# Kernel tuning notes

Measured on AMD Instinct MI355X. Metric: run time of the kernel, lower is better.

## Reference

```python
import jax, jax.numpy as jnp
import numpy as np
import math

N, E, G = 16000, 128000, 64
D, H, O, L, HID = 64, 4, 64, 5, 128
EPS = 1e-5

def _ln(x, g, b):
    mu = x.mean(-1, keepdims=True)
    var = ((x - mu) ** 2).mean(-1, keepdims=True)
    return (x - mu) / jnp.sqrt(var + EPS) * g + b

def _softplus_b64(x):
    # torch nn.Softplus(beta=64, threshold=64): x if 64*x > 64 else log1p(exp(64*x))/64
    z = jnp.minimum(x * 64.0, 64.0)
    return jnp.where(x * 64.0 > 64.0, x, jnp.log1p(jnp.exp(z)) / 64.0)

def setup_inputs() -> dict:
    key = jax.random.key(0)
    ks = jax.random.split(key, 32)
    s = 0.05
    d = {
        'x': jax.random.normal(ks[0], (N, 4), jnp.float32),
        'edge_attr': jax.random.normal(ks[1], (E, 9), jnp.float32),
        'edge_index': jax.random.randint(ks[2], (2, E), 0, N),
        'batch': jnp.sort(jax.random.randint(ks[3], (N,), 0, G)),
        'W_atom': jax.random.normal(ks[4], (4, D)) * s, 'b_atom': jnp.zeros((D,)),
        'We1': jax.random.normal(ks[5], (9, D)) * s, 'be1': jnp.zeros((D,)),
        'We2': jax.random.normal(ks[6], (D, D)) * s, 'be2': jnp.zeros((D,)),
        'Wq': jax.random.normal(ks[7], (L, D, H * O)) * s, 'bq': jnp.zeros((L, H * O)),
        'Wk': jax.random.normal(ks[8], (L, D, H * O)) * s, 'bk': jnp.zeros((L, H * O)),
        'Wv': jax.random.normal(ks[9], (L, D, H * O)) * s, 'bv': jnp.zeros((L, H * O)),
        'Wedge': jax.random.normal(ks[10], (L, D, H * O)) * s, 'bedge': jnp.zeros((L, H * O)),
        'Wfea': jax.random.normal(ks[11], (L, D, O)) * s, 'bfea': jnp.zeros((L, O)),
        'Wcat': jax.random.normal(ks[12], (L, H * O, O)) * s, 'bcat': jnp.zeros((L, O)),
        'Wupd': jax.random.normal(ks[13], (L, 3 * O, 3 * O)) * s, 'bupd': jnp.zeros((L, 3 * O)),
        'Wmsg': jax.random.normal(ks[14], (L, 3 * O, O)) * s, 'bmsg': jnp.zeros((L, O)),
        'g_msg': jnp.ones((L, O)), 'be_msg': jnp.zeros((L, O)),
        'g_ln': jnp.ones((L, 3 * O)), 'be_ln': jnp.zeros((L, 3 * O)),
        'g_bn': jnp.ones((L, O)), 'be_bn': jnp.zeros((L, O)),
        'Wfc': jax.random.normal(ks[15], (D, HID)) * s, 'bfc': jnp.zeros((HID,)),
        'Wout': jax.random.normal(ks[16], (HID, 1)) * s, 'bout': jnp.zeros((1,)),
    }
    return d

def _forward(x, edge_attr, W_atom, b_atom, We1, be1, We2, be2, Wq, bq, Wk, bk, Wv, bv,
             Wedge, bedge, Wfea, bfea, Wcat, bcat, Wupd, bupd, Wmsg, bmsg,
             g_msg, be_msg, g_ln, be_ln, g_bn, be_bn, Wfc, bfc, Wout, bout,
             edge_index, batch):
    src, dst = edge_index[0], edge_index[1]  # x_j = src, x_i = dst (flow source_to_target)
    h = x @ W_atom + b_atom  # [N, D]
    e = _softplus_b64(edge_attr @ We1 + be1) @ We2 + be2  # [E, D]
    scale = 1.0 / math.sqrt(3.0 * O)
    for l in range(L):
        Q = (h @ Wq[l] + bq[l]).reshape(N, H, O)
        K = (h @ Wk[l] + bk[l]).reshape(N, H, O)
        V = (h @ Wv[l] + bv[l]).reshape(N, H, O)
        Eh = (e @ Wedge[l] + bedge[l]).reshape(E, H, O)
        Qi = Q[dst]
        q_ij = jnp.concatenate([Qi, Qi, Qi], axis=-1)                 # [E, H, 3O]
        k_ij = jnp.concatenate([K[dst], K[src], Eh], axis=-1)
        v_ij = jnp.concatenate([V[dst], V[src], Eh], axis=-1)
        alpha = q_ij * k_ij * scale
        gate = jax.nn.sigmoid(_ln(alpha, g_ln[l], be_ln[l]))
        m = gate * (v_ij @ Wupd[l] + bupd[l])
        m = _ln(m @ Wmsg[l] + bmsg[l], g_msg[l], be_msg[l])           # [E, H, O]
        agg = jax.ops.segment_sum(m, dst, num_segments=N).reshape(N, H * O)
        out = agg @ Wcat[l] + bcat[l]
        mu = out.mean(0)
        var = ((out - mu) ** 2).mean(0)  # biased var, BN training mode
        out = (out - mu) / jnp.sqrt(var + EPS) * g_bn[l] + be_bn[l]
        h = jax.nn.silu(out) + (h @ Wfea[l] + bfea[l])
    ones = jnp.ones((N,), h.dtype)
    cnt = jax.ops.segment_sum(ones, batch, num_segments=G)
    pooled = jax.ops.segment_sum(h, batch, num_segments=G) / jnp.maximum(cnt, 1.0)[:, None]
    z = jax.nn.silu(pooled @ Wfc + bfc)
    return z @ Wout + bout  # [G, 1]

def reference(x, edge_attr, edge_index, batch, W_atom, b_atom, We1, be1, We2, be2,
              Wq, bq, Wk, bk, Wv, bv, Wedge, bedge, Wfea, bfea, Wcat, bcat,
              Wupd, bupd, Wmsg, bmsg, g_msg, be_msg, g_ln, be_ln, g_bn, be_bn,
              Wfc, bfc, Wout, bout):
    return _forward(x, edge_attr, W_atom, b_atom, We1, be1, We2, be2, Wq, bq, Wk, bk,
                    Wv, bv, Wedge, bedge, Wfea, bfea, Wcat, bcat, Wupd, bupd,
                    Wmsg, bmsg, g_msg, be_msg, g_ln, be_ln, g_bn, be_bn,
                    Wfc, bfc, Wout, bout, edge_index, batch)
```

## Files before the change

kernel.cpp:

```cpp
#include <hip/hip_runtime.h>
#include <hip/hip_bf16.h>
#include <math.h>

#define N_NODES 16000
#define N_EDGES 128000
#define N_GRAPH 64
#define NL 5
#define EPSV 1e-5f
#define SCALE 0.07216878364870323f

#define PCK 2048
#define ECOLS 1024
#define TILE 16
#define SWZ(r) (((r) & 7) << 2)

typedef __hip_bfloat16 bf16;
typedef __attribute__((ext_vector_type(8))) short short8;
typedef __attribute__((ext_vector_type(4))) short s4v;
typedef __attribute__((ext_vector_type(4))) float f32x4;
union S8U { short8 v; s4v h[2]; };

__device__ __forceinline__ ushort f2b(float x) {
    union { float f; uint u; } v; v.f = x;
    uint r = v.u + 0x7fffu + ((v.u >> 16) & 1u);
    return (ushort)(r >> 16);
}
__device__ __forceinline__ float b2fu(ushort u) { union { uint u; float f; } v; v.u = (uint)u << 16; return v.f; }
__device__ __forceinline__ float b2f_lo32(uint u) { union { uint u; float f; } v; v.u = u << 16; return v.f; }
__device__ __forceinline__ float b2f_hi32(uint u) { union { uint u; float f; } v; v.u = u & 0xffff0000u; return v.f; }

__global__ void pack_w(const float* __restrict__ Wq, const float* __restrict__ Wk,
                       const float* __restrict__ Wv, const float* __restrict__ Wupd,
                       const float* __restrict__ Wedge,
                       short* __restrict__ Wnp, short* __restrict__ Wep) {
    int idx = blockIdx.x * 256 + threadIdx.x;
    int total = NL * 64 * (PCK + ECOLS);
    if (idx >= total) return;
    int c = idx % (PCK + ECOLS);
    int k = (idx / (PCK + ECOLS)) % 64;
    int l = idx / (64 * (PCK + ECOLS));
    if (c < PCK) {
        int blk = c >> 10, hd = (c >> 8) & 3, ch = (c >> 2) & 63, j = c & 3;
        float v;
        if (blk == 0) {
            if (j == 0) v = Wq[(l*64 + k)*256 + hd*64 + ch];
            else {
                int p = (j - 1)*64 + ch;
                float s = 0.f;
                for (int q = 0; q < 64; ++q)
                    s += Wv[(l*64 + k)*256 + hd*64 + q] * Wupd[(l*192 + q)*192 + p];
                v = s;
            }
        } else {
            if (j == 0) v = Wk[(l*64 + k)*256 + hd*64 + ch];
            else {
                int p = (j - 1)*64 + ch;
                float s = 0.f;
                for (int q = 0; q < 64; ++q)
                    s += Wv[(l*64 + k)*256 + hd*64 + q] * Wupd[(l*192 + 64 + q)*192 + p];
                v = s;
            }
        }
        int t = c >> 4, s = k >> 5, lane = (c & 15) | (((k & 31) >> 3) << 4), jj = k & 7;
        size_t fo = ((size_t)(t*2 + s)*64 + lane)*8 + jj;
        ushort hi = f2b(v);
        ushort lo = f2b(v - b2fu(hi));
        Wnp[(size_t)l*2*64*PCK + fo] = (short)hi;
        Wnp[(size_t)l*2*64*PCK + (size_t)64*PCK + fo] = (short)lo;
    } else {
        int ce = c - PCK;
        float v;
        if (ce < 256) v = Wedge[(l*64 + k)*256 + ce];
        else {
            int cc = ce - 256, hd = cc / 192, p = cc % 192;
            float s = 0.f;
            for (int q = 0; q < 64; ++q)
                s += Wedge[(l*64 + k)*256 + hd*64 + q] * Wupd[(l*192 + 128 + q)*192 + p];
            v = s;
        }
        int t = ce >> 4, s = k >> 5, lane = (ce & 15) | (((k & 31) >> 3) << 4), jj = k & 7;
        size_t fo = ((size_t)(t*2 + s)*64 + lane)*8 + jj;
        ushort hi = f2b(v);
        ushort lo = f2b(v - b2fu(hi));
        Wep[(size_t)l*2*64*ECOLS + fo] = (short)hi;
        Wep[(size_t)l*2*64*ECOLS + (size_t)64*ECOLS + fo] = (short)lo;
    }
}

__global__ void pack_wmsg(const float* __restrict__ Wmsg, short* __restrict__ Wmf) {
    int idx = blockIdx.x * 256 + threadIdx.x;
    if (idx >= NL*192*64) return;
    int col = idx & 63, k = (idx >> 6) % 192, l = idx / (192*64);
    float v = Wmsg[(size_t)(l*192 + k)*64 + col];
    int t = col >> 4, s = k >> 5, lane = (col & 15) | (((k & 31) >> 3) << 4), j = k & 7;
    size_t fo = ((size_t)((t*6 + s)*64) + lane)*8 + j;
    ushort hi = f2b(v);
    ushort lo = f2b(v - b2fu(hi));
    Wmf[(size_t)l*2*12288 + fo] = (short)hi;
    Wmf[(size_t)l*2*12288 + 12288 + fo] = (short)lo;
}

__global__ void pack_b(const float* __restrict__ bq, const float* __restrict__ bk,
                       const float* __restrict__ bv, const float* __restrict__ Wupd,
                       const float* __restrict__ bupd, const float* __restrict__ bedge,
                       float* __restrict__ bnp, float* __restrict__ bep) {
    int idx = blockIdx.x * 256 + threadIdx.x;
    int total = NL * (PCK + ECOLS);
    if (idx >= total) return;
    int c = idx % (PCK + ECOLS);
    int l = idx / (PCK + ECOLS);
    if (c < PCK) {
        int blk = c >> 10, hd = (c >> 8) & 3, ch = (c >> 2) & 63, j = c & 3;
        float v;
        if (blk == 0) {
            if (j == 0) v = bq[l*256 + hd*64 + ch];
            else {
                int p = (j - 1)*64 + ch;
                float s = 0.f;
                for (int k = 0; k < 64; ++k) s += bv[l*256 + hd*64 + k] * Wupd[(l*192 + k)*192 + p];
                v = s;
            }
        } else {
            if (j == 0) v = bk[l*256 + hd*64 + ch];
            else {
                int p = (j - 1)*64 + ch;
                float s = 0.f;
                for (int k = 0; k < 64; ++k) s += bv[l*256 + hd*64 + k] * Wupd[(l*192 + 64 + k)*192 + p];
                v = s;
            }
        }
        bnp[l*PCK + c] = v;
    } else {
        int ce = c - PCK;
        float v;
        if (ce < 256) v = bedge[l*256 + ce];
        else {
            int cc = ce - 256, hd = cc / 192, p = cc % 192;
            float s = bupd[l*192 + p];
            for (int k = 0; k < 64; ++k) s += bedge[l*256 + hd*64 + k] * Wupd[(l*192 + 128 + k)*192 + p];
            v = s;
        }
        bep[l*ECOLS + ce] = v;
    }
}

__global__ void hist_k(const int* __restrict__ ei, int* __restrict__ hist) {
    int e = blockIdx.x * 256 + threadIdx.x;
    if (e < N_EDGES) atomicAdd(&hist[ei[N_EDGES + e]], 1);
}

__global__ void scan_k(const int* __restrict__ hist, int* __restrict__ binCur) {
    __shared__ int sBuf[256];
    __shared__ int sCarry;
    int tid = threadIdx.x;
    if (tid == 0) sCarry = 0;
    __syncthreads();
    for (int base = 0; base < N_NODES; base += 256) {
        int v = (base + tid < N_NODES) ? hist[base + tid] : 0;
        sBuf[tid] = v; __syncthreads();
        #pragma unroll
        for (int ofs = 1; ofs < 256; ofs <<= 1) {
            int t = (tid >= ofs) ? sBuf[tid - ofs] : 0;
            __syncthreads();
            sBuf[tid] += t;
            __syncthreads();
        }
        if (base + tid < N_NODES) binCur[base + tid] = sCarry + sBuf[tid] - v;
        __syncthreads();
        if (tid == 0) sCarry += sBuf[255];
        __syncthreads();
    }
}

__global__ void scatter_k(const int* __restrict__ ei, int* __restrict__ binCur,
                          int* __restrict__ perm, int* __restrict__ srcs, int* __restrict__ dsts) {
    int e = blockIdx.x * 256 + threadIdx.x;
    if (e < N_EDGES) {
        int d = ei[N_EDGES + e];
        int pos = atomicAdd(&binCur[d], 1);
        perm[pos] = e;
        srcs[pos] = ei[e];
        dsts[pos] = d;
    }
}

__global__ void init_h(const float* __restrict__ x, const float* __restrict__ W_atom,
                       const float* __restrict__ b_atom, float* __restrict__ h) {
    int idx = blockIdx.x * 256 + threadIdx.x;
    int d = idx & 63, n = idx >> 6;
    float s = b_atom[d];
    #pragma unroll
    for (int j = 0; j < 4; ++j) s += x[n*4 + j] * W_atom[j*64 + d];
    h[idx] = s;
}

__global__ void init_e(const float* __restrict__ ea, const float* __restrict__ We1,
                       const float* __restrict__ be1, const float* __restrict__ We2,
                       const float* __restrict__ be2, float* __restrict__ ef) {
    __shared__ float sT[4][64];
    int tid = threadIdx.x, d = tid & 63, sub = tid >> 6;
    int e = blockIdx.x * 4 + sub;
    float s = be1[d];
    #pragma unroll
    for (int j = 0; j < 9; ++j) s += ea[e*9 + j] * We1[j*64 + d];
    float x64 = s * 64.f;
    float sp = (x64 > 64.f) ? s : log1pf(__expf(fminf(x64, 64.f))) * (1.f/64.f);
    sT[sub][d] = sp;
    float acc = be2[d];
    #pragma unroll
    for (int k = 0; k < 64; ++k) acc += sT[sub][k] * We2[k*64 + d];
    ef[(size_t)e*64 + d] = acc;
}

__global__ void ef_frag(const float* __restrict__ ef, const int* __restrict__ perm,
                        ushort* __restrict__ efA) {
    int b = blockIdx.x, lane = threadIdx.x;
    int ep = perm[b*16 + (lane & 15)];
    const float* ar = ef + (size_t)ep*64 + ((lane >> 4) << 3);
    ushort* out = efA + (size_t)b*2048;
    #pragma unroll
    for (int s = 0; s < 2; ++s) {
        #pragma unroll
        for (int j = 0; j < 8; ++j) {
            float v = ar[s*32 + j];
            ushort hi = f2b(v);
            ushort lo = f2b(v - b2fu(hi));
            out[s*512 + lane*8 + j] = hi;
            out[1024 + s*512 + lane*8 + j] = lo;
        }
    }
}

#define CPAD 260
__global__ __launch_bounds__(256, 8) void proj_mfma(
    const float* __restrict__ A, const short* __restrict__ Whi, const short* __restrict__ Wlo,
    const float* __restrict__ bias, ushort* __restrict__ out, int M) {
    __shared__ short aHi[2*64*8];
    __shared__ short aLo[2*64*8];
    __shared__ ushort cTile[16*CPAD];
    int tid = threadIdx.x;
    int row0 = blockIdx.y * 16;
    int col0 = blockIdx.x * 256;
    {
        int r = tid >> 4, k0 = (tid & 15) * 4;
        const float4 v = *(const float4*)(A + (size_t)(row0 + r)*64 + k0);
        int s = k0 >> 5, lane = r | (((k0 & 31) >> 3) << 4), j0 = k0 & 7;
        ushort4 hb, lb;
        hb.x = f2b(v.x); lb.x = f2b(v.x - b2fu(hb.x));
        hb.y = f2b(v.y); lb.y = f2b(v.y - b2fu(hb.y));
        hb.z = f2b(v.z); lb.z = f2b(v.z - b2fu(hb.z));
        hb.w = f2b(v.w); lb.w = f2b(v.w - b2fu(hb.w));
        *(ushort4*)&aHi[(s*64 + lane)*8 + j0] = hb;
        *(ushort4*)&aLo[(s*64 + lane)*8 + j0] = lb;
    }
    __syncthreads();
    int w = tid >> 6, lane = tid & 63;
    short8 a0h = *(const short8*)&aHi[(0*64 + lane)*8];
    short8 a1h = *(const short8*)&aHi[(1*64 + lane)*8];
    short8 a0l = *(const short8*)&aLo[(0*64 + lane)*8];
    short8 a1l = *(const short8*)&aLo[(1*64 + lane)*8];
    int cl = lane & 15, rg = lane >> 4;
    #pragma unroll
    for (int nt = 0; nt < 4; ++nt) {
        int t = (col0 >> 4) + w*4 + nt;
        const short* bph = Whi + ((size_t)(t*2)*64 + lane)*8;
        const short* bpl = Wlo + ((size_t)(t*2)*64 + lane)*8;
        short8 b0h = *(const short8*)bph;
        short8 b1h = *(const short8*)(bph + 64*8);
        short8 b0l = *(const short8*)bpl;
        short8 b1l = *(const short8*)(bpl + 64*8);
        f32x4 acc = {0.f, 0.f, 0.f, 0.f};
        acc = __builtin_amdgcn_mfma_f32_16x16x32_bf16(a0h, b0h, acc, 0, 0, 0);
        acc = __builtin_amdgcn_mfma_f32_16x16x32_bf16(a1h, b1h, acc, 0, 0, 0);
        acc = __builtin_amdgcn_mfma_f32_16x16x32_bf16(a0l, b0h, acc, 0, 0, 0);
        acc = __builtin_amdgcn_mfma_f32_16x16x32_bf16(a1l, b1h, acc, 0, 0, 0);
        acc = __builtin_amdgcn_mfma_f32_16x16x32_bf16(a0h, b0l, acc, 0, 0, 0);
        acc = __builtin_amdgcn_mfma_f32_16x16x32_bf16(a1h, b1l, acc, 0, 0, 0);
        int ccol = w*64 + nt*16 + cl;
        float bv = bias[col0 + ccol];
        #pragma unroll
        for (int r = 0; r < 4; ++r)
            cTile[(rg*4 + r)*CPAD + ccol] = f2b(acc[r] + bv);
    }
    __syncthreads();
    {
        int r = tid >> 4, cs = (tid & 15) * 16;
        ushort* dst = out + (size_t)(row0 + r)*M + col0 + cs;
        const ushort* srcp = &cTile[r*CPAD + cs];
        #pragma unroll
        for (int q = 0; q < 4; ++q)
            *(ushort4*)(dst + q*4) = *(const ushort4*)(srcp + q*4);
    }
}

__global__ __launch_bounds__(256) void hf_proj(const float* __restrict__ h,
                                               const float* __restrict__ Wfea,
                                               const float* __restrict__ bfea,
                                               float* __restrict__ HF) {
    __shared__ float sW[64*64];
    __shared__ __align__(16) float sA[4][64];
    int tid = threadIdx.x;
    for (int i = tid; i < 4096; i += 256) sW[i] = Wfea[i];
    int c = tid & 63, no = tid >> 6;
    int n0 = blockIdx.x * 4;
    sA[no][c] = h[(size_t)(n0 + no)*64 + c];
    __syncthreads();
    float acc = bfea[c];
    #pragma unroll
    for (int k4 = 0; k4 < 16; ++k4) {
        float4 av = *(const float4*)&sA[no][k4*4];
        acc += av.x*sW[(k4*4+0)*64+c] + av.y*sW[(k4*4+1)*64+c]
             + av.z*sW[(k4*4+2)*64+c] + av.w*sW[(k4*4+3)*64+c];
    }
    HF[(size_t)(n0 + no)*64 + c] = acc;
}

__global__ __launch_bounds__(256, 5) void edge_fused(
    const ushort* __restrict__ Pu, const ushort* __restrict__ efA,
    const short* __restrict__ Wef, const float* __restrict__ bef,
    const int* __restrict__ srcs, const int* __restrict__ dsts,
    const short* __restrict__ Wmf, const float* __restrict__ bmsg,
    const float* __restrict__ g_ln, const float* __restrict__ be_ln,
    const float* __restrict__ g_msg, const float* __restrict__ be_msg,
    float* __restrict__ agg) {
    __shared__ __align__(16) ushort scr[4][TILE][256];
    int tid = threadIdx.x, lane = tid & 63, hd = tid >> 6;
    int e0 = blockIdx.x * TILE;
    int cl = lane & 15, rg = lane >> 4;
    {
        const ushort* fa = efA + (size_t)blockIdx.x * 2048;
        short8 a0h = *(const short8*)(fa + lane*8);
        short8 a1h = *(const short8*)(fa + 512 + lane*8);
        short8 a0l = *(const short8*)(fa + 1024 + lane*8);
        short8 a1l = *(const short8*)(fa + 1536 + lane*8);
        #pragma unroll
        for (int tt = 0; tt < 16; ++tt) {
            int tg = (tt < 4) ? (hd*4 + tt) : (16 + hd*12 + (tt - 4));
            const short* bph = Wef + ((size_t)(tg*2)*64 + lane)*8;
            const short* bpl = bph + (size_t)64*ECOLS;
            short8 b0h = *(const short8*)bph;
            short8 b1h = *(const short8*)(bph + 512);
            short8 b0l = *(const short8*)bpl;
            short8 b1l = *(const short8*)(bpl + 512);
            float bv = bef[tg*16 + cl];
            f32x4 acc = {bv, bv, bv, bv};
            acc = __builtin_amdgcn_mfma_f32_16x16x32_bf16(a0h, b0h, acc, 0, 0, 0);
            acc = __builtin_amdgcn_mfma_f32_16x16x32_bf16(a1h, b1h, acc, 0, 0, 0);
            acc = __builtin_amdgcn_mfma_f32_16x16x32_bf16(a0l, b0h, acc, 0, 0, 0);
            acc = __builtin_amdgcn_mfma_f32_16x16x32_bf16(a1l, b1h, acc, 0, 0, 0);
            acc = __builtin_amdgcn_mfma_f32_16x16x32_bf16(a0h, b0l, acc, 0, 0, 0);
            acc = __builtin_amdgcn_mfma_f32_16x16x32_bf16(a1h, b1l, acc, 0, 0, 0);
            int wcol = (tt < 4) ? (tt*16 + cl) : (64 + (tt - 4)*16 + cl);
            #pragma unroll
            for (int r = 0; r < 4; ++r) {
                int row = rg*4 + r;
                scr[hd][row][wcol ^ SWZ(row)] = f2b(acc[r]);
            }
        }
    }
    float gl0 = g_ln[lane], gl1 = g_ln[64 + lane], gl2 = g_ln[128 + lane];
    float bl0 = be_ln[lane], bl1 = be_ln[64 + lane], bl2 = be_ln[128 + lane];
    int prevDst = -1;
    uint2 D = {0, 0}, Kd = {0, 0};
    #pragma unroll 4
    for (int it = 0; it < TILE; ++it) {
        int xw = SWZ(it);
        int src = srcs[e0 + it], dst = dsts[e0 + it];
        if (dst != prevDst) {
            D  = *(const uint2*)(Pu + (size_t)dst*PCK + hd*256 + (lane << 2));
            Kd = *(const uint2*)(Pu + (size_t)dst*PCK + 1024 + hd*256 + (lane << 2));
            prevDst = dst;
        }
        const uint2 S = *(const uint2*)(Pu + (size_t)src*PCK + 1024 + hd*256 + (lane << 2));
        float q   = b2f_lo32(D.x),  vd0 = b2f_hi32(D.x);
        float vd1 = b2f_lo32(D.y),  vd2 = b2f_hi32(D.y);
        float kd  = b2f_lo32(Kd.x);
        float ks  = b2f_lo32(S.x),  vs0 = b2f_hi32(S.x);
        float vs1 = b2f_lo32(S.y),  vs2 = b2f_hi32(S.y);
        float eh = b2fu(scr[hd][it][lane ^ xw]);
        float a0 = q*kd*SCALE, a1 = q*ks*SCALE, a2 = q*eh*SCALE;
        float s = a0 + a1 + a2, ss = a0*a0 + a1*a1 + a2*a2;
        #pragma unroll
        for (int m = 1; m < 64; m <<= 1) { s += __shfl_xor(s, m); ss += __shfl_xor(ss, m); }
        float mu = s * (1.f/192.f);
        float var = ss * (1.f/192.f) - mu*mu;
        float rstd = rsqrtf(var + EPSV);
        float g0 = __builtin_amdgcn_rcpf(1.f + __expf(-((a0 - mu)*rstd*gl0 + bl0)));
        float g1 = __builtin_amdgcn_rcpf(1.f + __expf(-((a1 - mu)*rstd*gl1 + bl1)));
        float g2 = __builtin_amdgcn_rcpf(1.f + __expf(-((a2 - mu)*rstd*gl2 + bl2)));
        float vu0 = vd0 + vs0 + b2fu(scr[hd][it][(64 + lane) ^ xw]);
        float vu1 = vd1 + vs1 + b2fu(scr[hd][it][(128 + lane) ^ xw]);
        float vu2 = vd2 + vs2 + b2fu(scr[hd][it][(192 + lane) ^ xw]);
        scr[hd][it][(64 + lane) ^ xw]  = f2b(g0*vu0);
        scr[hd][it][(128 + lane) ^ xw] = f2b(g1*vu1);
        scr[hd][it][(192 + lane) ^ xw] = f2b(g2*vu2);
    }
    float bmsv[4], gmv[4], bmv[4];
    #pragma unroll
    for (int t = 0; t < 4; ++t) {
        bmsv[t] = bmsg[t*16 + cl];
        gmv[t]  = g_msg[t*16 + cl];
        bmv[t]  = be_msg[t*16 + cl];
    }
    int dstr[4];
    #pragma unroll
    for (int r = 0; r < 4; ++r) dstr[r] = dsts[e0 + rg*4 + r];
    f32x4 acc[4];
    #pragma unroll
    for (int t = 0; t < 4; ++t) acc[t] = (f32x4){bmsv[t], bmsv[t], bmsv[t], bmsv[t]};
    #pragma unroll
    for (int s = 0; s < 6; ++s) {
        S8U a;
        int c0 = 64 + s*32 + rg*8, xs = SWZ(cl);
        a.h[0] = *(const s4v*)&scr[hd][cl][c0 ^ xs];
        a.h[1] = *(const s4v*)&scr[hd][cl][(c0 + 4) ^ xs];
        #pragma unroll
        for (int t = 0; t < 4; ++t) {
            const short* bp = &Wmf[((size_t)((t*6 + s)*64) + lane)*8];
            short8 bh = *(const short8*)bp;
            short8 bl = *(const short8*)(bp + 12288);
            acc[t] = __builtin_amdgcn_mfma_f32_16x16x32_bf16(a.v, bh, acc[t], 0, 0, 0);
            acc[t] = __builtin_amdgcn_mfma_f32_16x16x32_bf16(a.v, bl, acc[t], 0, 0, 0);
        }
    }
    float nv[4][4];
    #pragma unroll
    for (int r = 0; r < 4; ++r) {
        float s1 = acc[0][r] + acc[1][r] + acc[2][r] + acc[3][r];
        float s2 = acc[0][r]*acc[0][r] + acc[1][r]*acc[1][r]
                 + acc[2][r]*acc[2][r] + acc[3][r]*acc[3][r];
        #pragma unroll
        for (int m = 1; m < 16; m <<= 1) { s1 += __shfl_xor(s1, m); s2 += __shfl_xor(s2, m); }
        float mu = s1 * (1.f/64.f);
        float var = s2 * (1.f/64.f) - mu*mu;
        float rstd = rsqrtf(var + EPSV);
        #pragma unroll
        for (int t = 0; t < 4; ++t) nv[t][r] = (acc[t][r] - mu)*rstd*gmv[t] + bmv[t];
    }
    int cur = dstr[0];
    float r0 = nv[0][0], r1 = nv[1][0], r2 = nv[2][0], r3 = nv[3][0];
    #pragma unroll
    for (int r = 1; r < 4; ++r) {
        if (dstr[r] == cur) {
            r0 += nv[0][r]; r1 += nv[1][r]; r2 += nv[2][r]; r3 += nv[3][r];
        } else {
            float* base = &agg[(size_t)cur*256 + hd*64];
            atomicAdd(base + 0*16 + cl, r0);
            atomicAdd(base + 1*16 + cl, r1);
            atomicAdd(base + 2*16 + cl, r2);
            atomicAdd(base + 3*16 + cl, r3);
            cur = dstr[r];
            r0 = nv[0][r]; r1 = nv[1][r]; r2 = nv[2][r]; r3 = nv[3][r];
        }
    }
    {
        float* base = &agg[(size_t)cur*256 + hd*64];
        atomicAdd(base + 0*16 + cl, r0);
        atomicAdd(base + 1*16 + cl, r1);
        atomicAdd(base + 2*16 + cl, r2);
        atomicAdd(base + 3*16 + cl, r3);
    }
}

__global__ __launch_bounds__(256, 2) void agg_out(
    const float* __restrict__ agg, const float* __restrict__ Wcat, const float* __restrict__ bcat,
    float* __restrict__ out, float* __restrict__ bnsum, float* __restrict__ bnss) {
    __shared__ float sW[256 * 64];
    __shared__ __align__(16) float sA[4][256];
    __shared__ float sR[4][64];
    int tid = threadIdx.x;
    for (int i = tid; i < 256*64; i += 256) sW[i] = Wcat[i];
    int c = tid & 63, no = tid >> 6;
    float bc = bcat[c];
    float psum = 0.f, psq = 0.f;
    __syncthreads();
    int nbase = blockIdx.x * 64;
    for (int it = 0; it < 16; ++it) {
        for (int i = tid; i < 1024; i += 256)
            sA[i >> 8][i & 255] = agg[(size_t)(nbase + it*4 + (i >> 8))*256 + (i & 255)];
        __syncthreads();
        float acc = bc;
        #pragma unroll
        for (int k4 = 0; k4 < 64; ++k4) {
            float4 av = *(const float4*)&sA[no][k4*4];
            acc += av.x*sW[(k4*4+0)*64 + c] + av.y*sW[(k4*4+1)*64 + c]
                 + av.z*sW[(k4*4+2)*64 + c] + av.w*sW[(k4*4+3)*64 + c];
        }
        out[(size_t)(nbase + it*4 + no)*64 + c] = acc;
        psum += acc; psq += acc*acc;
        __syncthreads();
    }
    sR[no][c] = psum; __syncthreads();
    if (no == 0) atomicAdd(&bnsum[c], sR[0][c] + sR[1][c] + sR[2][c] + sR[3][c]);
    __syncthreads();
    sR[no][c] = psq; __syncthreads();
    if (no == 0) atomicAdd(&bnss[c], sR[0][c] + sR[1][c] + sR[2][c] + sR[3][c]);
}

__global__ void bn_silu(const float* __restrict__ out, const float* __restrict__ HF,
                        const float* __restrict__ bnsum, const float* __restrict__ bnss,
                        const float* __restrict__ g_bn, const float* __restrict__ be_bn,
                        float* __restrict__ h) {
    int idx = blockIdx.x * 256 + threadIdx.x;
    int c = idx & 63;
    float mu = bnsum[c] * (1.f/N_NODES);
    float var = bnss[c] * (1.f/N_NODES) - mu*mu;
    float rstd = rsqrtf(var + EPSV);
    float v = (out[idx] - mu)*rstd*g_bn[c] + be_bn[c];
    float sv = v / (1.f + __expf(-v));
    h[idx] = sv + HF[idx];
}

__device__ __forceinline__ int lbound(const int* __restrict__ a, int n, int v) {
    int lo = 0, hi = n;
    while (lo < hi) { int m = (lo + hi) >> 1; if (a[m] < v) lo = m + 1; else hi = m; }
    return lo;
}

__global__ __launch_bounds__(256) void pool_head(
    const float* __restrict__ h, const int* __restrict__ batch,
    const float* __restrict__ Wfc, const float* __restrict__ bfc,
    const float* __restrict__ Wout, const float* __restrict__ bout,
    float* __restrict__ d_out) {
    __shared__ float sPart[4][64];
    __shared__ float sP[64];
    __shared__ float red[128];
    int g = blockIdx.x, tid = threadIdx.x;
    int lo = lbound(batch, N_NODES, g);
    int hi = lbound(batch, N_NODES, g + 1);
    int c = tid & 63, rg = tid >> 6;
    float s = 0.f;
    for (int n = lo + rg; n < hi; n += 4) s += h[(size_t)n*64 + c];
    sPart[rg][c] = s;
    __syncthreads();
    if (tid < 64)
        sP[tid] = (sPart[0][tid] + sPart[1][tid] + sPart[2][tid] + sPart[3][tid])
                  * (1.f / fmaxf((float)(hi - lo), 1.f));
    __syncthreads();
    if (tid < 128) {
        float acc = bfc[tid];
        #pragma unroll
        for (int k = 0; k < 64; ++k) acc += sP[k] * Wfc[k*128 + tid];
        float z = acc / (1.f + __expf(-acc));
        red[tid] = z * Wout[tid];
    }
    __syncthreads();
    for (int s1 = 64; s1 > 0; s1 >>= 1) {
        if (tid < s1 && tid + s1 < 128) red[tid] += red[tid + s1];
        __syncthreads();
    }
    if (tid == 0) d_out[g] = red[0] + bout[0];
}

extern "C" void kernel_launch(void* const* d_in, const int* in_sizes, int n_in,
                              void* d_out, int out_size, void* d_ws, size_t ws_size,
                              hipStream_t stream) {
    const float* x        = (const float*)d_in[0];
    const float* edge_attr= (const float*)d_in[1];
    const int*   ei       = (const int*)  d_in[2];
    const int*   batch    = (const int*)  d_in[3];
    const float* W_atom=(const float*)d_in[4];  const float* b_atom=(const float*)d_in[5];
    const float* We1  =(const float*)d_in[6];   const float* be1  =(const float*)d_in[7];
    const float* We2  =(const float*)d_in[8];   const float* be2  =(const float*)d_in[9];
    const float* Wq   =(const float*)d_in[10];  const float* bq   =(const float*)d_in[11];
    const float* Wk   =(const float*)d_in[12];  const float* bk   =(const float*)d_in[13];
    const float* Wv   =(const float*)d_in[14];  const float* bv   =(const float*)d_in[15];
    const float* Wedge=(const float*)d_in[16];  const float* bedge=(const float*)d_in[17];
    const float* Wfea =(const float*)d_in[18];  const float* bfea =(const float*)d_in[19];
    const float* Wcat =(const float*)d_in[20];  const float* bcat =(const float*)d_in[21];
    const float* Wupd =(const float*)d_in[22];  const float* bupd =(const float*)d_in[23];
    const float* Wmsg =(const float*)d_in[24];  const float* bmsg =(const float*)d_in[25];
    const float* g_msg=(const float*)d_in[26];  const float* be_msg=(const float*)d_in[27];
    const float* g_ln =(const float*)d_in[28];  const float* be_ln=(const float*)d_in[29];
    const float* g_bn =(const float*)d_in[30];  const float* be_bn=(const float*)d_in[31];
    const float* Wfc  =(const float*)d_in[32];  const float* bfc  =(const float*)d_in[33];
    const float* Wout =(const float*)d_in[34];  const float* bout =(const float*)d_in[35];

    char* ws = (char*)d_ws;
    size_t off = 0;
    auto alloc = [&](size_t bytes) {
        void* p = ws + off;
        off += (bytes + 255) & ~(size_t)255;
        return p;
    };
    short* Wnp  = (short*)alloc((size_t)NL*2*64*PCK*2);
    float* bnp  = (float*)alloc((size_t)NL*PCK*4);
    short* Wep  = (short*)alloc((size_t)NL*2*64*ECOLS*2);
    float* bep  = (float*)alloc((size_t)NL*ECOLS*4);
    short* Wmf  = (short*)alloc((size_t)NL*2*12288*2);
    float* h    = (float*)alloc((size_t)N_NODES*64*4);
    float* ef   = (float*)alloc((size_t)N_EDGES*64*4);
    ushort* efA = (ushort*)alloc((size_t)(N_EDGES/TILE)*2048*2);
    ushort* P   = (ushort*)alloc((size_t)N_NODES*PCK*2);
    float* HF   = (float*)alloc((size_t)N_NODES*64*4);
    float* agg  = (float*)alloc((size_t)N_NODES*256*4);
    float* outb = (float*)alloc((size_t)N_NODES*64*4);
    float* bnsum= (float*)alloc(64*4);
    float* bnss = (float*)alloc(64*4);
    int* histB  = (int*)alloc((size_t)N_NODES*4);
    int* binCur = (int*)alloc((size_t)N_NODES*4);
    int* perm   = (int*)alloc((size_t)N_EDGES*4);
    int* srcs   = (int*)alloc((size_t)N_EDGES*4);
    int* dsts   = (int*)alloc((size_t)N_EDGES*4);
    if (off > ws_size) return;

    {
        int total = NL*64*(PCK+ECOLS);
        pack_w<<<(total+255)/256, 256, 0, stream>>>(Wq, Wk, Wv, Wupd, Wedge, Wnp, Wep);
        int tb = NL*(PCK+ECOLS);
        pack_b<<<(tb+255)/256, 256, 0, stream>>>(bq, bk, bv, Wupd, bupd, bedge, bnp, bep);
        pack_wmsg<<<(NL*192*64+255)/256, 256, 0, stream>>>(Wmsg, Wmf);
    }
    hipMemsetAsync(histB, 0, (size_t)N_NODES*4, stream);
    hist_k<<<(N_EDGES+255)/256, 256, 0, stream>>>(ei, histB);
    scan_k<<<1, 256, 0, stream>>>(histB, binCur);
    scatter_k<<<(N_EDGES+255)/256, 256, 0, stream>>>(ei, binCur, perm, srcs, dsts);

    init_h<<<(N_NODES*64)/256, 256, 0, stream>>>(x, W_atom, b_atom, h);
    init_e<<<N_EDGES/4, 256, 0, stream>>>(edge_attr, We1, be1, We2, be2, ef);
    ef_frag<<<N_EDGES/TILE, 64, 0, stream>>>(ef, perm, efA);

    for (int l = 0; l < NL; ++l) {
        const short* Wh = Wnp + (size_t)l*2*64*PCK;
        proj_mfma<<<dim3(PCK/256, N_NODES/16), 256, 0, stream>>>(
            h, Wh, Wh + (size_t)64*PCK, bnp + l*PCK, P, PCK);
        hf_proj<<<N_NODES/4, 256, 0, stream>>>(h, Wfea + (size_t)l*64*64, bfea + l*64, HF);
        hipMemsetAsync(agg, 0, (size_t)N_NODES*256*4, stream);
        hipMemsetAsync(bnsum, 0, 64*4, stream);
        hipMemsetAsync(bnss, 0, 64*4, stream);
        edge_fused<<<N_EDGES/TILE, 256, 0, stream>>>(
            P, efA, Wep + (size_t)l*2*64*ECOLS, bep + l*ECOLS, srcs, dsts,
            Wmf + (size_t)l*2*12288, bmsg + l*64,
            g_ln + l*192, be_ln + l*192, g_msg + l*64, be_msg + l*64, agg);
        agg_out<<<N_NODES/64, 256, 0, stream>>>(agg, Wcat + (size_t)l*256*64, bcat + l*64,
                                                outb, bnsum, bnss);
        bn_silu<<<(N_NODES*64)/256, 256, 0, stream>>>(outb, HF, bnsum, bnss,
                                                      g_bn + l*64, be_bn + l*64, h);
    }
    pool_head<<<N_GRAPH, 256, 0, stream>>>(h, batch, Wfc, bfc, Wout, bout, (float*)d_out);
}
```

Before: 1.844 ms.

## Replace scalar FP32 node GEMMs with split-bf16 MFMA row kernel

Swaps the scalar FP32 hf_proj and agg_out matmuls for one generic row_mfma kernel. It splits the fp32 activations and packed weights into bf16 hi/lo pairs and runs three MFMA products to keep near-fp32 accuracy, folding the BN sum and sum-of-squares into per-wave shuffles and atomics. New pack_rw kernels pre-pack Wcat and Wfea into the MFMA fragment layout. Separately, several edge_fused bf16 stores switch to the library __float2bfloat16 conversion instead of the hand-rolled rounding. The aim is to cut ALU and LDS cost in the per-layer node GEMMs, in exchange for more BN-statistic atomics (one per wave) and slight numerical differences.

```diff
diff --git a/kernel.cpp b/kernel.cpp
--- a/kernel.cpp
+++ b/kernel.cpp
@@ -24,6 +24,10 @@
     union { float f; uint u; } v; v.f = x;
     uint r = v.u + 0x7fffu + ((v.u >> 16) & 1u);
     return (ushort)(r >> 16);
+}
+__device__ __forceinline__ ushort f2b_n(float x) {
+    union { bf16 b; ushort u; } v; v.b = __float2bfloat16(x);
+    return v.u;
 }
 __device__ __forceinline__ float b2fu(ushort u) { union { uint u; float f; } v; v.u = (uint)u << 16; return v.f; }
 __device__ __forceinline__ float b2f_lo32(uint u) { union { uint u; float f; } v; v.u = u << 16; return v.f; }
@@ -100,6 +104,21 @@
     Wmf[(size_t)l*2*12288 + 12288 + fo] = (short)lo;
 }
 
+__global__ void pack_rw(const float* __restrict__ W, short* __restrict__ Wf, int K) {
+    int idx = blockIdx.x * 256 + threadIdx.x;
+    if (idx >= NL*K*64) return;
+    int col = idx & 63, k = (idx >> 6) % K, l = idx / (K*64);
+    float v = W[(size_t)(l*K + k)*64 + col];
+    int t = col >> 4, s = k >> 5, lane = (col & 15) | (((k & 31) >> 3) << 4), j = k & 7;
+    int nks = K >> 5;
+    size_t plane = (size_t)nks * 2048;
+    size_t fo = ((size_t)((t*nks + s)*64) + lane)*8 + j;
+    ushort hi = f2b(v);
+    ushort lo = f2b(v - b2fu(hi));
+    Wf[(size_t)l*2*plane + fo] = (short)hi;
+    Wf[(size_t)l*2*plane + plane + fo] = (short)lo;
+}
+
 __global__ void pack_b(const float* __restrict__ bq, const float* __restrict__ bk,
                        const float* __restrict__ bv, const float* __restrict__ Wupd,
                        const float* __restrict__ bupd, const float* __restrict__ bedge,
@@ -293,26 +312,60 @@
     }
 }
 
-__global__ __launch_bounds__(256) void hf_proj(const float* __restrict__ h,
-                                               const float* __restrict__ Wfea,
-                                               const float* __restrict__ bfea,
-                                               float* __restrict__ HF) {
-    __shared__ float sW[64*64];
-    __shared__ __align__(16) float sA[4][64];
+__global__ __launch_bounds__(256, 4) void row_mfma(
+    const float* __restrict__ A, const short* __restrict__ Wf, const float* __restrict__ bias,
+    float* __restrict__ out, int nks, float* __restrict__ bnsum, float* __restrict__ bnss) {
+    __shared__ short aHi[8*64*8];
+    __shared__ short aLo[8*64*8];
     int tid = threadIdx.x;
-    for (int i = tid; i < 4096; i += 256) sW[i] = Wfea[i];
-    int c = tid & 63, no = tid >> 6;
-    int n0 = blockIdx.x * 4;
-    sA[no][c] = h[(size_t)(n0 + no)*64 + c];
+    int row0 = blockIdx.x * 16;
+    int K = nks << 5;
+    int cpt = K >> 4;
+    {
+        int r = tid >> 4, c0 = (tid & 15) * cpt;
+        const float* ap = A + (size_t)(row0 + r)*K + c0;
+        for (int q = 0; q < cpt; q += 4) {
+            float4 v = *(const float4*)(ap + q);
+            ushort4 hb, lb;
+            hb.x = f2b(v.x); lb.x = f2b(v.x - b2fu(hb.x));
+            hb.y = f2b(v.y); lb.y = f2b(v.y - b2fu(hb.y));
+            hb.z = f2b(v.z); lb.z = f2b(v.z - b2fu(hb.z));
+            hb.w = f2b(v.w); lb.w = f2b(v.w - b2fu(hb.w));
+            int k = c0 + q;
+            int s = k >> 5, lane = r | (((k & 31) >> 3) << 4), jj = k & 7;
+            *(ushort4*)&aHi[(s*64 + lane)*8 + jj] = hb;
+            *(ushort4*)&aLo[(s*64 + lane)*8 + jj] = lb;
+        }
+    }
     __syncthreads();
-    float acc = bfea[c];
-    #pragma unroll
-    for (int k4 = 0; k4 < 16; ++k4) {
-        float4 av = *(const float4*)&sA[no][k4*4];
-        acc += av.x*sW[(k4*4+0)*64+c] + av.y*sW[(k4*4+1)*64+c]
-             + av.z*sW[(k4*4+2)*64+c] + av.w*sW[(k4*4+3)*64+c];
-    }
-    HF[(size_t)(n0 + no)*64 + c] = acc;
+    int w = tid >> 6, lane = tid & 63;
+    int cl = lane & 15, rg = lane >> 4;
+    size_t plane = (size_t)nks * 2048;
+    f32x4 acc = {0.f, 0.f, 0.f, 0.f};
+    for (int s = 0; s < nks; ++s) {
+        short8 ah = *(const short8*)&aHi[(s*64 + lane)*8];
+        short8 al = *(const short8*)&aLo[(s*64 + lane)*8];
+        const short* bp = Wf + ((size_t)((w*nks + s)*64) + lane)*8;
+        short8 bh = *(const short8*)bp;
+        short8 bl = *(const short8*)(bp + plane);
+        acc = __builtin_amdgcn_mfma_f32_16x16x32_bf16(ah, bh, acc, 0, 0, 0);
+        acc = __builtin_amdgcn_mfma_f32_16x16x32_bf16(al, bh, acc, 0, 0, 0);
+        acc = __builtin_amdgcn_mfma_f32_16x16x32_bf16(ah, bl, acc, 0, 0, 0);
+    }
+    int col = w*16 + cl;
+    float bc = bias[col];
+    float psum = 0.f, psq = 0.f;
+    #pragma unroll
+    for (int r2 = 0; r2 < 4; ++r2) {
+        float v = acc[r2] + bc;
+        out[(size_t)(row0 + rg*4 + r2)*64 + col] = v;
+        psum += v; psq += v*v;
+    }
+    if (bnsum) {
+        psum += __shfl_xor(psum, 16); psum += __shfl_xor(psum, 32);
+        psq  += __shfl_xor(psq, 16);  psq  += __shfl_xor(psq, 32);
+        if (rg == 0) { atomicAdd(&bnsum[col], psum); atomicAdd(&bnss[col], psq); }
+    }
 }
 
 __global__ __launch_bounds__(256, 5) void edge_fused(
@@ -354,7 +407,7 @@
             #pragma unroll
             for (int r = 0; r < 4; ++r) {
                 int row = rg*4 + r;
-                scr[hd][row][wcol ^ SWZ(row)] = f2b(acc[r]);
+                scr[hd][row][wcol ^ SWZ(row)] = f2b_n(acc[r]);
             }
         }
     }
@@ -391,9 +444,9 @@
         float vu0 = vd0 + vs0 + b2fu(scr[hd][it][(64 + lane) ^ xw]);
         float vu1 = vd1 + vs1 + b2fu(scr[hd][it][(128 + lane) ^ xw]);
         float vu2 = vd2 + vs2 + b2fu(scr[hd][it][(192 + lane) ^ xw]);
-        scr[hd][it][(64 + lane) ^ xw]  = f2b(g0*vu0);
-        scr[hd][it][(128 + lane) ^ xw] = f2b(g1*vu1);
-        scr[hd][it][(192 + lane) ^ xw] = f2b(g2*vu2);
+        scr[hd][it][(64 + lane) ^ xw]  = f2b_n(g0*vu0);
+        scr[hd][it][(128 + lane) ^ xw] = f2b_n(g1*vu1);
+        scr[hd][it][(192 + lane) ^ xw] = f2b_n(g2*vu2);
     }
     float bmsv[4], gmv[4], bmv[4];
     #pragma unroll
@@ -460,41 +513,6 @@
         atomicAdd(base + 2*16 + cl, r2);
         atomicAdd(base + 3*16 + cl, r3);
     }
-}
-
-__global__ __launch_bounds__(256, 2) void agg_out(
-    const float* __restrict__ agg, const float* __restrict__ Wcat, const float* __restrict__ bcat,
-    float* __restrict__ out, float* __restrict__ bnsum, float* __restrict__ bnss) {
-    __shared__ float sW[256 * 64];
-    __shared__ __align__(16) float sA[4][256];
-    __shared__ float sR[4][64];
-    int tid = threadIdx.x;
-    for (int i = tid; i < 256*64; i += 256) sW[i] = Wcat[i];
-    int c = tid & 63, no = tid >> 6;
-    float bc = bcat[c];
-    float psum = 0.f, psq = 0.f;
-    __syncthreads();
-    int nbase = blockIdx.x * 64;
-    for (int it = 0; it < 16; ++it) {
-        for (int i = tid; i < 1024; i += 256)
-            sA[i >> 8][i & 255] = agg[(size_t)(nbase + it*4 + (i >> 8))*256 + (i & 255)];
-        __syncthreads();
-        float acc = bc;
-        #pragma unroll
-        for (int k4 = 0; k4 < 64; ++k4) {
-            float4 av = *(const float4*)&sA[no][k4*4];
-            acc += av.x*sW[(k4*4+0)*64 + c] + av.y*sW[(k4*4+1)*64 + c]
-                 + av.z*sW[(k4*4+2)*64 + c] + av.w*sW[(k4*4+3)*64 + c];
-        }
-        out[(size_t)(nbase + it*4 + no)*64 + c] = acc;
-        psum += acc; psq += acc*acc;
-        __syncthreads();
-    }
-    sR[no][c] = psum; __syncthreads();
-    if (no == 0) atomicAdd(&bnsum[c], sR[0][c] + sR[1][c] + sR[2][c] + sR[3][c]);
-    __syncthreads();
-    sR[no][c] = psq; __syncthreads();
-    if (no == 0) atomicAdd(&bnss[c], sR[0][c] + sR[1][c] + sR[2][c] + sR[3][c]);
 }
 
 __global__ void bn_silu(const float* __restrict__ out, const float* __restrict__ HF,
@@ -588,6 +606,8 @@
     short* Wep  = (short*)alloc((size_t)NL*2*64*ECOLS*2);
     float* bep  = (float*)alloc((size_t)NL*ECOLS*4);
     short* Wmf  = (short*)alloc((size_t)NL*2*12288*2);
+    short* Wcf  = (short*)alloc((size_t)NL*2*16384*2);
+    short* Wff  = (short*)alloc((size_t)NL*2*4096*2);
     float* h    = (float*)alloc((size_t)N_NODES*64*4);
     float* ef   = (float*)alloc((size_t)N_EDGES*64*4);
     ushort* efA = (ushort*)alloc((size_t)(N_EDGES/TILE)*2048*2);
@@ -610,6 +630,8 @@
         int tb = NL*(PCK+ECOLS);
         pack_b<<<(tb+255)/256, 256, 0, stream>>>(bq, bk, bv, Wupd, bupd, bedge, bnp, bep);
         pack_wmsg<<<(NL*192*64+255)/256, 256, 0, stream>>>(Wmsg, Wmf);
+        pack_rw<<<(NL*256*64+255)/256, 256, 0, stream>>>(Wcat, Wcf, 256);
+        pack_rw<<<(NL*64*64+255)/256, 256, 0, stream>>>(Wfea, Wff, 64);
     }
     hipMemsetAsync(histB, 0, (size_t)N_NODES*4, stream);
     hist_k<<<(N_EDGES+255)/256, 256, 0, stream>>>(ei, histB);
@@ -624,7 +646,8 @@
         const short* Wh = Wnp + (size_t)l*2*64*PCK;
         proj_mfma<<<dim3(PCK/256, N_NODES/16), 256, 0, stream>>>(
             h, Wh, Wh + (size_t)64*PCK, bnp + l*PCK, P, PCK);
-        hf_proj<<<N_NODES/4, 256, 0, stream>>>(h, Wfea + (size_t)l*64*64, bfea + l*64, HF);
+        row_mfma<<<N_NODES/16, 256, 0, stream>>>(
+            h, Wff + (size_t)l*2*4096, bfea + l*64, HF, 2, nullptr, nullptr);
         hipMemsetAsync(agg, 0, (size_t)N_NODES*256*4, stream);
         hipMemsetAsync(bnsum, 0, 64*4, stream);
         hipMemsetAsync(bnss, 0, 64*4, stream);
@@ -632,8 +655,8 @@
             P, efA, Wep + (size_t)l*2*64*ECOLS, bep + l*ECOLS, srcs, dsts,
             Wmf + (size_t)l*2*12288, bmsg + l*64,
             g_ln + l*192, be_ln + l*192, g_msg + l*64, be_msg + l*64, agg);
-        agg_out<<<N_NODES/64, 256, 0, stream>>>(agg, Wcat + (size_t)l*256*64, bcat + l*64,
-                                                outb, bnsum, bnss);
+        row_mfma<<<N_NODES/16, 256, 0, stream>>>(
+            agg, Wcf + (size_t)l*2*16384, bcat + l*64, outb, 8, bnsum, bnss);
         bn_silu<<<(N_NODES*64)/256, 256, 0, stream>>>(outb, HF, bnsum, bnss,
                                                       g_bn + l*64, be_bn + l*64, h);
     }
```

Result: faster. 1.699 ms (-7.9%).
